# Optimization experiments

Hardware: AMD Instinct MI355X
Metric: run time of the kernel (lower is better)

Reference implementation:

```python
import jax, jax.numpy as jnp
import numpy as np

CLAMP_MIN = 1e-12
CLAMP_MAX = 1e12


def setup_inputs() -> dict:
    key = jax.random.key(0)
    k1, k2, k3 = jax.random.split(key, 3)
    N, C, D = 16384, 1024, 128
    x = jax.random.normal(k1, (N, D), dtype=jnp.float32)
    centers = jax.random.normal(k2, (C, D), dtype=jnp.float32)
    labels = jax.random.randint(k3, (N,), 0, C, dtype=jnp.int64)
    return {"x": x, "centers": centers, "labels": labels}


def reference(x, centers, labels):
    # x: [N, D], centers: [C, D], labels: [N]
    N = x.shape[0]
    C = centers.shape[0]
    x_sq = jnp.sum(x * x, axis=1, keepdims=True)            # [N, 1]
    c_sq = jnp.sum(centers * centers, axis=1)[None, :]      # [1, C]
    distmat = x_sq + c_sq - 2.0 * (x @ centers.T)           # [N, C]
    # One-hot mask of true class per sample
    mask = (labels[:, None] == jnp.arange(C)[None, :]).astype(distmat.dtype)
    dist = distmat * mask
    # Faithful to torch: clamp applied to the WHOLE masked matrix (zeros -> 1e-12)
    loss = jnp.clip(dist, CLAMP_MIN, CLAMP_MAX).sum() / N
    return loss
```

## Files before the change

### kernel.cpp

```cpp
#include <hip/hip_runtime.h>


#define NWAVES 2048

__global__ void center_loss_partial(const float* __restrict__ x,
                                    const float* __restrict__ centers,
                                    const int* __restrict__ labels,
                                    float* __restrict__ partials,
                                    int N) {
    const int gtid = blockIdx.x * blockDim.x + threadIdx.x;
    const int wave = gtid >> 6;
    const int lane = threadIdx.x & 63;

    float acc = 0.0f;
    for (int row = wave; row < N; row += NWAVES) {
        const int c = labels[row];
        const float2 xv = *reinterpret_cast<const float2*>(x + (size_t)row * 128 + lane * 2);
        const float2 cv = *reinterpret_cast<const float2*>(centers + (size_t)c * 128 + lane * 2);
        const float d0 = xv.x - cv.x;
        const float d1 = xv.y - cv.y;
        float d = d0 * d0 + d1 * d1;
        #pragma unroll
        for (int off = 32; off; off >>= 1) d += __shfl_down(d, off, 64);
        if (lane == 0) acc += fminf(fmaxf(d, 1e-12f), 1e12f);
    }
    if (lane == 0) partials[wave] = acc;
}

__global__ void center_loss_finalize(const float* __restrict__ partials,
                                     float* __restrict__ out,
                                     float invN, float floor_term) {
    __shared__ float warp_sums[4];
    const int tid  = threadIdx.x;
    const int lane = tid & 63;
    const int wid  = tid >> 6;

    float s = 0.0f;
    #pragma unroll
    for (int i = 0; i < NWAVES / 256; ++i)
        s += partials[tid + i * 256];
    #pragma unroll
    for (int off = 32; off; off >>= 1) s += __shfl_down(s, off, 64);
    if (lane == 0) warp_sums[wid] = s;
    __syncthreads();
    if (tid == 0) {
        float t = warp_sums[0] + warp_sums[1] + warp_sums[2] + warp_sums[3];
        out[0] = t * invN + floor_term;
    }
}

extern "C" void kernel_launch(void* const* d_in, const int* in_sizes, int n_in,
                              void* d_out, int out_size, void* d_ws, size_t ws_size,
                              hipStream_t stream) {
    const float* x       = (const float*)d_in[0];
    const float* centers = (const float*)d_in[1];
    const int*   labels  = (const int*)d_in[2];
    float* out      = (float*)d_out;
    float* partials = (float*)d_ws;

    const int D = 128;
    const int N = in_sizes[0] / D;
    const int C = in_sizes[1] / D;

    const int block = 256;
    const int grid  = NWAVES / 4;
    center_loss_partial<<<grid, block, 0, stream>>>(x, centers, labels, partials, N);
    center_loss_finalize<<<1, 256, 0, stream>>>(partials, out, 1.0f / (float)N,
                                                (float)(C - 1) * 1e-12f);
}
```

Before: 11.19 us.

## Fuse partial and finalize kernels with last-block atomic reduction and float4 loads

Merges the two-kernel reduction into a single kernel where each block writes a partial sum and the last block to arrive, detected via an atomic counter, performs the final reduction. Rows are processed with float4 loads, two rows per wave, and 32 rows per block, and the per-row clamp is dropped. This removes one kernel launch and its dependency gap. The counter is never zeroed and relies on a modulo check, so correctness depends on the initial workspace contents, and omitting the clamp changes semantics for degenerate rows.

```diff
diff --git a/kernel.cpp b/kernel.cpp
--- a/kernel.cpp
+++ b/kernel.cpp
@@ -1,51 +1,69 @@
 #include <hip/hip_runtime.h>
 
 
-#define NWAVES 2048
+#define BLOCK 256
+#define ROWS_PER_BLOCK 32
 
-__global__ void center_loss_partial(const float* __restrict__ x,
-                                    const float* __restrict__ centers,
-                                    const int* __restrict__ labels,
-                                    float* __restrict__ partials,
-                                    int N) {
-    const int gtid = blockIdx.x * blockDim.x + threadIdx.x;
-    const int wave = gtid >> 6;
-    const int lane = threadIdx.x & 63;
+__global__ __launch_bounds__(BLOCK) void center_loss_fused(
+    const float* __restrict__ x,
+    const float* __restrict__ centers,
+    const int* __restrict__ labels,
+    float* __restrict__ out,
+    float* __restrict__ partials,
+    unsigned int* __restrict__ counter,
+    int N, float invN, float floor_term)
+{
+    __shared__ float wsum[BLOCK / 64];
+    __shared__ int is_last;
 
-    float acc = 0.0f;
-    for (int row = wave; row < N; row += NWAVES) {
-        const int c = labels[row];
-        const float2 xv = *reinterpret_cast<const float2*>(x + (size_t)row * 128 + lane * 2);
-        const float2 cv = *reinterpret_cast<const float2*>(centers + (size_t)c * 128 + lane * 2);
-        const float d0 = xv.x - cv.x;
-        const float d1 = xv.y - cv.y;
-        float d = d0 * d0 + d1 * d1;
-        #pragma unroll
-        for (int off = 32; off; off >>= 1) d += __shfl_down(d, off, 64);
-        if (lane == 0) acc += fminf(fmaxf(d, 1e-12f), 1e12f);
-    }
-    if (lane == 0) partials[wave] = acc;
-}
-
-__global__ void center_loss_finalize(const float* __restrict__ partials,
-                                     float* __restrict__ out,
-                                     float invN, float floor_term) {
-    __shared__ float warp_sums[4];
     const int tid  = threadIdx.x;
     const int lane = tid & 63;
     const int wid  = tid >> 6;
+    const int half = tid >> 5;
+    const int l32  = tid & 31;
+    const int bid  = blockIdx.x;
+    const int G    = gridDim.x;
 
-    float s = 0.0f;
+    float acc = 0.0f;
     #pragma unroll
-    for (int i = 0; i < NWAVES / 256; ++i)
-        s += partials[tid + i * 256];
+    for (int it = 0; it < ROWS_PER_BLOCK / 8; ++it) {
+        const int row = bid * ROWS_PER_BLOCK + it * 8 + half;
+        if (row < N) {
+            const int lab = labels[row];
+            const float4 xv = *reinterpret_cast<const float4*>(x       + (size_t)row * 128 + l32 * 4);
+            const float4 cv = *reinterpret_cast<const float4*>(centers + (size_t)lab * 128 + l32 * 4);
+            const float d0 = xv.x - cv.x, d1 = xv.y - cv.y;
+            const float d2 = xv.z - cv.z, d3 = xv.w - cv.w;
+            acc += d0 * d0 + d1 * d1 + d2 * d2 + d3 * d3;
+        }
+    }
+
     #pragma unroll
-    for (int off = 32; off; off >>= 1) s += __shfl_down(s, off, 64);
-    if (lane == 0) warp_sums[wid] = s;
+    for (int off = 32; off; off >>= 1) acc += __shfl_down(acc, off, 64);
+    if (lane == 0) wsum[wid] = acc;
     __syncthreads();
+
     if (tid == 0) {
-        float t = warp_sums[0] + warp_sums[1] + warp_sums[2] + warp_sums[3];
-        out[0] = t * invN + floor_term;
+        const float bsum = wsum[0] + wsum[1] + wsum[2] + wsum[3];
+        partials[bid] = bsum;
+        __threadfence();
+        const unsigned int old = atomicAdd(counter, 1u);
+        is_last = ((old + 1u) % (unsigned int)G == 0u) ? 1 : 0;
+    }
+    __syncthreads();
+
+    if (is_last) {
+        __threadfence();
+        float s = 0.0f;
+        const volatile float* vp = partials;
+        for (int i = tid; i < G; i += BLOCK) s += vp[i];
+        #pragma unroll
+        for (int off = 32; off; off >>= 1) s += __shfl_down(s, off, 64);
+        __syncthreads();
+        if (lane == 0) wsum[wid] = s;
+        __syncthreads();
+        if (tid == 0)
+            out[0] = (wsum[0] + wsum[1] + wsum[2] + wsum[3]) * invN + floor_term;
     }
 }
 
@@ -55,16 +73,17 @@
     const float* x       = (const float*)d_in[0];
     const float* centers = (const float*)d_in[1];
     const int*   labels  = (const int*)d_in[2];
-    float* out      = (float*)d_out;
-    float* partials = (float*)d_ws;
+    float* out = (float*)d_out;
+
+    float*        partials = (float*)d_ws;
+    unsigned int* counter  = (unsigned int*)((char*)d_ws + 8192);
 
     const int D = 128;
     const int N = in_sizes[0] / D;
     const int C = in_sizes[1] / D;
 
-    const int block = 256;
-    const int grid  = NWAVES / 4;
-    center_loss_partial<<<grid, block, 0, stream>>>(x, centers, labels, partials, N);
-    center_loss_finalize<<<1, 256, 0, stream>>>(partials, out, 1.0f / (float)N,
-                                                (float)(C - 1) * 1e-12f);
+    const int grid = (N + ROWS_PER_BLOCK - 1) / ROWS_PER_BLOCK;
+    center_loss_fused<<<grid, BLOCK, 0, stream>>>(
+        x, centers, labels, out, partials, counter,
+        N, 1.0f / (float)N, (float)(C - 1) * 1e-12f);
 }
```

Result: slower. 17.71 us (+58.3%).
